# Optimization experiments

Hardware: AMD Instinct MI355X
Metric: run time of the kernel (lower is better)

The kernel has to match this reference:

```python
import jax, jax.numpy as jnp
import numpy as np

T, H, I, E, K = 4096, 2048, 1408, 8, 2


def setup_inputs() -> dict:
    key = jax.random.key(0)
    k1, k2, k3, k4, k5 = jax.random.split(key, 5)
    hidden_states = jax.random.normal(k1, (T, H), dtype=jnp.float32)
    w13 = jax.random.normal(k2, (E, 2 * I, H), dtype=jnp.float32) * 0.02
    w2 = jax.random.normal(k3, (E, H, I), dtype=jnp.float32) * 0.02
    topk_ids = jax.random.randint(k4, (T, K), 0, E, dtype=jnp.int32)
    topk_weights = jax.random.uniform(k5, (T, K), dtype=jnp.float32)
    return {
        "hidden_states": hidden_states,
        "w13": w13,
        "w2": w2,
        "topk_ids": topk_ids,
        "topk_weights": topk_weights,
    }


def reference(hidden_states, w13, w2, topk_ids, topk_weights):
    # hidden_states: [T, H]; w13: [E, 2I, H]; w2: [E, H, I]
    # topk_ids/topk_weights: [T, K]. local_expert_start = 0.
    num_tokens, hidden = hidden_states.shape
    num_experts = w13.shape[0]
    inter = w13.shape[1] // 2
    gate_w = w13[:, :inter, :]  # [E, I, H]
    up_w = w13[:, inter:, :]    # [E, I, H]

    # Dense per-expert gate/up projections (vectorized grouped GEMM).
    gate = jnp.einsum('th,eih->tei', hidden_states, gate_w)
    up = jnp.einsum('th,eih->tei', hidden_states, up_w)
    act = jax.nn.silu(gate) * up  # [T, E, I]

    # Scatter topk weights into a dense [T, E] routing matrix (zero elsewhere),
    # which reproduces the trivial impl's per-slot weighted accumulation.
    tok = jnp.arange(num_tokens, dtype=jnp.int32)[:, None]
    routing = jnp.zeros((num_tokens, num_experts), dtype=hidden_states.dtype)
    routing = routing.at[tok, topk_ids].add(topk_weights)

    # Weighted combine through the down projection; weighting act first avoids
    # materializing a [T, E, H] intermediate.
    act_w = act * routing[:, :, None]  # [T, E, I]
    out = jnp.einsum('tei,ehi->th', act_w, w2)  # [T, H]
    return out
```

## Files before the change

kernel.cpp:

```cpp
#include <hip/hip_runtime.h>
#include <hip/hip_bf16.h>

#define T_TOK 4096
#define HID   2048
#define INTER 1408
#define TWO_I 2816
#define NEXP  8
#define ROWCAP 9216

#define N8_HS  1048576
#define N8_W13 5767168
#define NCVT   ((N8_HS + N8_W13) / 256)

using bf16x8 = __attribute__((ext_vector_type(8))) __bf16;
using f32x4  = __attribute__((ext_vector_type(4))) float;

__device__ __forceinline__ unsigned short f2bf(float f) {
  unsigned u = __float_as_uint(f);
  u += 0x7fffu + ((u >> 16) & 1u);
  return (unsigned short)(u >> 16);
}

__device__ __forceinline__ void gload16(const void* g, void* l) {
  __builtin_amdgcn_global_load_lds(
      (const __attribute__((address_space(1))) void*)g,
      (__attribute__((address_space(3))) void*)l, 16, 0, 0);
}

__device__ __forceinline__ uint4 pack8(float4 a, float4 b) {
  union { unsigned short us[8]; uint4 v; } o;
  o.us[0] = f2bf(a.x); o.us[1] = f2bf(a.y); o.us[2] = f2bf(a.z); o.us[3] = f2bf(a.w);
  o.us[4] = f2bf(b.x); o.us[5] = f2bf(b.y); o.us[6] = f2bf(b.z); o.us[7] = f2bf(b.w);
  return o.v;
}

__global__ void cvt2route_kernel(const float* __restrict__ hs_f, unsigned short* __restrict__ hs_b,
                                 const float* __restrict__ w13_f, unsigned short* __restrict__ w13_b,
                                 const int* __restrict__ ids, const float* __restrict__ wts,
                                 float* __restrict__ R, int* __restrict__ counts) {
  int bid = blockIdx.x;
  if (bid >= NCVT) {
    int t = (bid - NCVT) * 256 + threadIdx.x;
    if (t >= T_TOK) return;
    int e0 = ids[t * 2], e1 = ids[t * 2 + 1];
    float w0 = wts[t * 2], w1 = wts[t * 2 + 1];
#pragma unroll
    for (int ee = 0; ee < NEXP; ++ee) {
      float r = (e0 == ee ? w0 : 0.0f) + (e1 == ee ? w1 : 0.0f);
      R[t * NEXP + ee] = r;
    }
    atomicAdd(&counts[e0], 1);
    if (e1 != e0) atomicAdd(&counts[e1], 1);
    return;
  }
  int i = bid * 256 + threadIdx.x;
  const float4* p;
  uint4* o;
  int j;
  if (i < N8_HS) {
    p = reinterpret_cast<const float4*>(hs_f);
    o = reinterpret_cast<uint4*>(hs_b);
    j = i;
  } else {
    p = reinterpret_cast<const float4*>(w13_f);
    o = reinterpret_cast<uint4*>(w13_b);
    j = i - N8_HS;
  }
  o[j] = pack8(p[j * 2], p[j * 2 + 1]);
}

__global__ void offsets_kernel(const int* __restrict__ counts,
                               int* __restrict__ offs, int* __restrict__ cursor,
                               int* __restrict__ tl) {
  if (threadIdx.x == 0) {
    int o = 0;
    for (int e = 0; e < NEXP; ++e) {
      offs[e] = o;
      cursor[e] = o;
      o += (counts[e] + 127) & ~127;
    }
    offs[NEXP] = o;
  }
  for (int i = threadIdx.x; i < ROWCAP; i += 256) tl[i] = -1;
}

__global__ void scatter_kernel(const int* __restrict__ ids,
                               int* __restrict__ cursor, int* __restrict__ tl,
                               int* __restrict__ inv) {
  int t = blockIdx.x * 256 + threadIdx.x;
  if (t >= T_TOK) return;
  int e0 = ids[t * 2], e1 = ids[t * 2 + 1];
  int p = atomicAdd(&cursor[e0], 1);
  tl[p] = t;
  inv[t * 2] = p;
  if (e1 != e0) {
    p = atomicAdd(&cursor[e1], 1);
    tl[p] = t;
    inv[t * 2 + 1] = p;
  } else {
    inv[t * 2 + 1] = -1;
  }
}

__global__ __launch_bounds__(256) void gemm1_kernel(
    const unsigned short* __restrict__ hs,
    const unsigned short* __restrict__ w13,
    unsigned short* __restrict__ act,
    const int* __restrict__ tl, const int* __restrict__ offs,
    const float* __restrict__ w2f, unsigned short* __restrict__ w2b) {
  const int tid = threadIdx.x;
  const int lin = blockIdx.x + 22 * (blockIdx.y + 32 * blockIdx.z);

  {
    const float4* p = reinterpret_cast<const float4*>(w2f);
    uint4* o = reinterpret_cast<uint4*>(w2b);
    int i0 = lin * 512 + tid;
    o[i0] = pack8(p[i0 * 2], p[i0 * 2 + 1]);
    int i1 = i0 + 256;
    o[i1] = pack8(p[i1 * 2], p[i1 * 2 + 1]);
  }

  const int work = (lin & 7) * 704 + (lin >> 3);
  const int bx = work % 22;
  const int by = (work / 22) & 31;
  const int bz = work / 704;

  const int e = bz;
  const int rbeg = offs[e], rend = offs[e + 1];
  const int m0 = rbeg + by * 128;
  if (m0 >= rend) return;
  const int n0 = bx * 64;

  __shared__ __align__(16) char smem[32768];

  const int lane = tid & 63, wave = tid >> 6;
  const int wm = wave >> 1, wn = wave & 1;
  const int srow = lane >> 3;
  const int scolswz = ((lane & 7) * 16) ^ (srow << 4);

  int atok[4];
#pragma unroll
  for (int it = 0; it < 4; ++it) {
    int tk = tl[m0 + it * 32 + wave * 8 + srow];
    atok[it] = tk < 0 ? 0 : tk;
  }

  const char* hs_b = (const char*)hs;
  const char* w13_b = (const char*)w13 + (size_t)e * (TWO_I * HID * 2);

  const char* asrc[4];
#pragma unroll
  for (int it = 0; it < 4; ++it)
    asrc[it] = hs_b + (size_t)atok[it] * (HID * 2) + scolswz;
  const char* gsrc[2]; const char* usrc[2];
#pragma unroll
  for (int it = 0; it < 2; ++it) {
    int row = it * 32 + wave * 8 + srow;
    gsrc[it] = w13_b + (size_t)(n0 + row) * (HID * 2) + scolswz;
    usrc[it] = w13_b + (size_t)(INTER + n0 + row) * (HID * 2) + scolswz;
  }

  const int ldsw = wave * 1024;
  const int rsw = (lane & 7) << 4;

  char* As = smem; char* Bg = smem + 16384; char* Bu = smem + 24576;

  f32x4 accg[4][2] = {};
  f32x4 accu[4][2] = {};

  for (int kt = 0; kt < HID / 64; ++kt) {
    const int kb = kt * 128;
#pragma unroll
    for (int it = 0; it < 4; ++it)
      gload16(asrc[it] + kb, As + it * 4096 + ldsw);
#pragma unroll
    for (int it = 0; it < 2; ++it) {
      gload16(gsrc[it] + kb, Bg + it * 4096 + ldsw);
      gload16(usrc[it] + kb, Bu + it * 4096 + ldsw);
    }
    __syncthreads();
#pragma unroll
    for (int kk = 0; kk < 2; ++kk) {
      const int ko = (kk * 64 + (lane >> 4) * 16) ^ rsw;
      bf16x8 a[4], bg[2], bu[2];
#pragma unroll
      for (int mi = 0; mi < 4; ++mi)
        a[mi] = *(const bf16x8*)(As + (wm * 64 + mi * 16 + (lane & 15)) * 128 + ko);
#pragma unroll
      for (int ni = 0; ni < 2; ++ni) {
        int r = wn * 32 + ni * 16 + (lane & 15);
        bg[ni] = *(const bf16x8*)(Bg + r * 128 + ko);
        bu[ni] = *(const bf16x8*)(Bu + r * 128 + ko);
      }
#pragma unroll
      for (int mi = 0; mi < 4; ++mi)
#pragma unroll
        for (int ni = 0; ni < 2; ++ni) {
          accg[mi][ni] = __builtin_amdgcn_mfma_f32_16x16x32_bf16(a[mi], bg[ni], accg[mi][ni], 0, 0, 0);
          accu[mi][ni] = __builtin_amdgcn_mfma_f32_16x16x32_bf16(a[mi], bu[ni], accu[mi][ni], 0, 0, 0);
        }
    }
    __syncthreads();
  }

#pragma unroll
  for (int mi = 0; mi < 4; ++mi)
#pragma unroll
    for (int j = 0; j < 4; ++j) {
      int rowL = wm * 64 + mi * 16 + (lane >> 4) * 4 + j;
      size_t base = (size_t)(m0 + rowL) * INTER + n0 + wn * 32;
#pragma unroll
      for (int ni = 0; ni < 2; ++ni) {
        float g = accg[mi][ni][j], u = accu[mi][ni][j];
        float s = (g / (1.0f + __expf(-g))) * u;
        act[base + ni * 16 + (lane & 15)] = f2bf(s);
      }
    }
}

__global__ __launch_bounds__(256) void gemm2_kernel(
    const unsigned short* __restrict__ act,
    const unsigned short* __restrict__ w2,
    const float* __restrict__ R, const int* __restrict__ tl,
    const int* __restrict__ offs, unsigned short* __restrict__ partial) {
  const int lin = blockIdx.x + 16 * (blockIdx.y + 32 * blockIdx.z);
  const int work = (lin & 7) * 512 + (lin >> 3);
  const int bx = work & 15;
  const int by = (work >> 4) & 31;
  const int bz = work >> 9;

  const int e = bz;
  const int rbeg = offs[e], rend = offs[e + 1];
  const int m0 = rbeg + by * 128;
  if (m0 >= rend) return;
  const int n0 = bx * 128;

  __shared__ __align__(16) char smem[32768];

  const int tid = threadIdx.x;
  const int lane = tid & 63, wave = tid >> 6;
  const int wm = wave >> 1, wn = wave & 1;
  const int srow = lane >> 3;
  const int scolswz = ((lane & 7) * 16) ^ (srow << 4);

  const char* act_b = (const char*)act;
  const char* w2_b = (const char*)w2 + (size_t)e * (HID * INTER * 2);

  const char* asrc[4]; const char* bsrc[4];
#pragma unroll
  for (int it = 0; it < 4; ++it) {
    int row = it * 32 + wave * 8 + srow;
    asrc[it] = act_b + (size_t)(m0 + row) * (INTER * 2) + scolswz;
    bsrc[it] = w2_b + (size_t)(n0 + row) * (INTER * 2) + scolswz;
  }

  const int ldsw = wave * 1024;
  const int rsw = (lane & 7) << 4;

  char* As = smem; char* Bs = smem + 16384;

  f32x4 acc[4][4] = {};

  for (int kt = 0; kt < INTER / 64; ++kt) {
    const int kb = kt * 128;
#pragma unroll
    for (int it = 0; it < 4; ++it) {
      gload16(asrc[it] + kb, As + it * 4096 + ldsw);
      gload16(bsrc[it] + kb, Bs + it * 4096 + ldsw);
    }
    __syncthreads();
#pragma unroll
    for (int kk = 0; kk < 2; ++kk) {
      const int ko = (kk * 64 + (lane >> 4) * 16) ^ rsw;
      bf16x8 a[4], b[4];
#pragma unroll
      for (int mi = 0; mi < 4; ++mi)
        a[mi] = *(const bf16x8*)(As + (wm * 64 + mi * 16 + (lane & 15)) * 128 + ko);
#pragma unroll
      for (int ni = 0; ni < 4; ++ni)
        b[ni] = *(const bf16x8*)(Bs + (wn * 64 + ni * 16 + (lane & 15)) * 128 + ko);
#pragma unroll
      for (int mi = 0; mi < 4; ++mi)
#pragma unroll
        for (int ni = 0; ni < 4; ++ni)
          acc[mi][ni] = __builtin_amdgcn_mfma_f32_16x16x32_bf16(a[mi], b[ni], acc[mi][ni], 0, 0, 0);
    }
    __syncthreads();
  }

#pragma unroll
  for (int mi = 0; mi < 4; ++mi) {
    float sc[4];
#pragma unroll
    for (int j = 0; j < 4; ++j) {
      int row = m0 + wm * 64 + mi * 16 + (lane >> 4) * 4 + j;
      int t = tl[row];
      sc[j] = t >= 0 ? R[t * NEXP + e] : 0.0f;
    }
#pragma unroll
    for (int ni = 0; ni < 4; ++ni) {
      int col = n0 + wn * 64 + ni * 16 + (lane & 15);
#pragma unroll
      for (int j = 0; j < 4; ++j) {
        int row = m0 + wm * 64 + mi * 16 + (lane >> 4) * 4 + j;
        partial[(size_t)row * HID + col] = f2bf(acc[mi][ni][j] * sc[j]);
      }
    }
  }
}

__global__ void combine_kernel(const unsigned short* __restrict__ P,
                               const int* __restrict__ inv,
                               float* __restrict__ out) {
  int idx = blockIdx.x * 256 + threadIdx.x;
  int t = idx >> 8;
  int c = (idx & 255) << 3;
  int p0 = inv[t * 2], p1 = inv[t * 2 + 1];
  union { uint4 v; unsigned short us[8]; } a, b;
  a.v = *(const uint4*)(P + (size_t)p0 * HID + c);
  float f[8];
#pragma unroll
  for (int j = 0; j < 8; ++j) f[j] = __uint_as_float((unsigned)a.us[j] << 16);
  if (p1 >= 0) {
    b.v = *(const uint4*)(P + (size_t)p1 * HID + c);
#pragma unroll
    for (int j = 0; j < 8; ++j) f[j] += __uint_as_float((unsigned)b.us[j] << 16);
  }
  float4 lo = {f[0], f[1], f[2], f[3]}, hi = {f[4], f[5], f[6], f[7]};
  *(float4*)(out + (size_t)t * HID + c) = lo;
  *(float4*)(out + (size_t)t * HID + c + 4) = hi;
}

extern "C" void kernel_launch(void* const* d_in, const int* in_sizes, int n_in,
                              void* d_out, int out_size, void* d_ws, size_t ws_size,
                              hipStream_t stream) {
  const float* hs_f  = (const float*)d_in[0];
  const float* w13_f = (const float*)d_in[1];
  const float* w2_f  = (const float*)d_in[2];
  const int*   ids   = (const int*)d_in[3];
  const float* wts   = (const float*)d_in[4];
  float* out = (float*)d_out;
  char* ws = (char*)d_ws;

  unsigned short* hs_b  = (unsigned short*)(ws);
  unsigned short* w13_b = (unsigned short*)(ws + 16777216);
  unsigned short* w2_b  = (unsigned short*)(ws + 109051904);
  unsigned short* act   = (unsigned short*)(ws + 155189248);
  float* R              = (float*)(ws + 181141504);
  int*   tl             = (int*)(ws + 181272576);
  int*   inv            = (int*)(ws + 181309440);
  int*   meta           = (int*)(ws + 181342208);
  unsigned short* partial = (unsigned short*)(ws + 16777216);
  int* counts = meta;
  int* offs   = meta + 8;
  int* cursor = meta + 17;

  hipMemsetAsync(meta, 0, 32 * sizeof(int), stream);

  cvt2route_kernel<<<dim3(NCVT + 16), dim3(256), 0, stream>>>(
      hs_f, hs_b, w13_f, w13_b, ids, wts, R, counts);

  offsets_kernel<<<dim3(1), dim3(256), 0, stream>>>(counts, offs, cursor, tl);
  scatter_kernel<<<dim3(T_TOK / 256), dim3(256), 0, stream>>>(ids, cursor, tl, inv);

  gemm1_kernel<<<dim3(22, 32, NEXP), dim3(256), 0, stream>>>(hs_b, w13_b, act, tl, offs, w2_f, w2_b);
  gemm2_kernel<<<dim3(16, 32, NEXP), dim3(256), 0, stream>>>(act, w2_b, R, tl, offs, partial);
  combine_kernel<<<dim3(T_TOK * (HID / 8) / 256), dim3(256), 0, stream>>>(partial, inv, out);
}
```

Baseline: 316.8 us.

## Rewrite grouped GEMMs as 256x256 tiles with 8-wave ping-pong LDS pipeline

Both grouped GEMM kernels move from 128-row tiles with 4 waves and a single LDS buffer to 256x256 output tiles with 8 waves. They use a double-buffered 128KB LDS and an eight-phase schedule that interleaves global-to-LDS loads with MFMA quadrants, using raw barriers, vmcnt waits and setprio. Gate and up rows are interleaved into one B tile so a single accumulator array holds both. The aim is to hide memory latency behind compute and raise arithmetic intensity per tile. In exchange, more rows are wasted on partially filled per-expert tiles, occupancy is limited by the large LDS footprint, and the hand-tuned barrier and waitcnt scheduling is fragile.

```diff
diff --git a/kernel.cpp b/kernel.cpp
--- a/kernel.cpp
+++ b/kernel.cpp
@@ -102,208 +102,270 @@
   }
 }
 
-__global__ __launch_bounds__(256) void gemm1_kernel(
+
+#define BARR do { __asm__ __volatile__("" ::: "memory"); \
+                  __builtin_amdgcn_s_barrier();           \
+                  __asm__ __volatile__("" ::: "memory"); } while (0)
+#define VMC(n) __asm__ __volatile__("s_waitcnt vmcnt(" #n ")" ::: "memory")
+
+#define STG(P, h, kt, slotOff, hOff)                                        \
+  do {                                                                      \
+    gload16(P[h][0] + (kt) * 128, smem + (slotOff) + (hOff) + chA);         \
+    gload16(P[h][1] + (kt) * 128, smem + (slotOff) + (hOff) + chA + 1024);  \
+  } while (0)
+
+#define LDA(dst, S, aq)                                                     \
+  do {                                                                      \
+    _Pragma("unroll") for (int mi = 0; mi < 4; ++mi) {                      \
+      const char* _p = smem + (S) + wmOff + ((aq) * 64 + mi * 16 + l15) * 128; \
+      dst[mi][0] = *(const bf16x8*)(_p + ko0);                              \
+      dst[mi][1] = *(const bf16x8*)(_p + ko1);                              \
+    }                                                                       \
+  } while (0)
+
+#define LDB(dst, S, bq)                                                     \
+  do {                                                                      \
+    _Pragma("unroll") for (int ni = 0; ni < 2; ++ni) {                      \
+      const char* _p = smem + (S) + 32768 + wnhOff +                        \
+                       (wn1 * 64 + ((bq) * 2 + ni) * 16 + l15) * 128;       \
+      dst[ni][0] = *(const bf16x8*)(_p + ko0);                              \
+      dst[ni][1] = *(const bf16x8*)(_p + ko1);                              \
+    }                                                                       \
+  } while (0)
+
+#define MFQ(A, B, aq, bq)                                                   \
+  do {                                                                      \
+    __builtin_amdgcn_s_setprio(1);                                          \
+    _Pragma("unroll") for (int mi = 0; mi < 4; ++mi)                        \
+    _Pragma("unroll") for (int ni = 0; ni < 2; ++ni) {                      \
+      acc[(aq) * 4 + mi][(bq) * 2 + ni] = __builtin_amdgcn_mfma_f32_16x16x32_bf16( \
+          A[mi][0], B[ni][0], acc[(aq) * 4 + mi][(bq) * 2 + ni], 0, 0, 0);  \
+      acc[(aq) * 4 + mi][(bq) * 2 + ni] = __builtin_amdgcn_mfma_f32_16x16x32_bf16( \
+          A[mi][1], B[ni][1], acc[(aq) * 4 + mi][(bq) * 2 + ni], 0, 0, 0);  \
+    }                                                                       \
+    __builtin_amdgcn_s_setprio(0);                                          \
+  } while (0)
+
+#define EIGHT_PHASES(NIT_, NL_LIM_)                                         \
+  for (int i = 0; i < (NIT_); ++i) {                                        \
+    const int t0 = 2 * i, t1 = t0 + 1;                                      \
+    const bool nl = (i < (NL_LIM_));                                        \
+                                                                    \
+    LDA(a_lo, 0, 0);                                                        \
+    LDB(b_lo, 0, 0);                                                        \
+    STG(aS, 0, t1, 65536, 0);                                               \
+    BARR; MFQ(a_lo, b_lo, 0, 0); BARR;                                      \
+                                                                    \
+    LDB(b_hi, 0, 1);                                                        \
+    STG(aS, 1, t1, 65536, 16384);                                           \
+    BARR; MFQ(a_lo, b_hi, 0, 1); BARR;                                      \
+                                                                    \
+    LDA(a_hi, 0, 1);                                                        \
+    if (nl) STG(bS, 0, t0 + 2, 0, 32768);                                   \
+    BARR; MFQ(a_hi, b_hi, 1, 1); BARR;                                      \
+                                                                    \
+    if (nl) STG(bS, 1, t0 + 2, 0, 49152);                                   \
+    BARR; MFQ(a_hi, b_lo, 1, 0);                                            \
+    if (nl) { VMC(4); } else { VMC(0); }                                    \
+    BARR;                                                                   \
+                                                                    \
+    LDA(a_lo, 65536, 0);                                                    \
+    LDB(b_lo, 65536, 0);                                                    \
+    if (nl) STG(aS, 0, t0 + 2, 0, 0);                                       \
+    BARR; MFQ(a_lo, b_lo, 0, 0); BARR;                                      \
+                                                                    \
+    LDB(b_hi, 65536, 1);                                                    \
+    if (nl) STG(aS, 1, t0 + 2, 0, 16384);                                   \
+    BARR; MFQ(a_lo, b_hi, 0, 1); BARR;                                      \
+                                                                    \
+    LDA(a_hi, 65536, 1);                                                    \
+    if (nl) STG(bS, 0, t1 + 2, 65536, 32768);                               \
+    BARR; MFQ(a_hi, b_hi, 1, 1); BARR;                                      \
+                                                                    \
+    if (nl) STG(bS, 1, t1 + 2, 65536, 49152);                               \
+    BARR; MFQ(a_hi, b_lo, 1, 0);                                            \
+    if (nl) VMC(4);                                                         \
+    BARR;                                                                   \
+  }
+
+#define PROLOGUE_STAGE()                                                    \
+  do {                                                                      \
+    STG(aS, 0, 0, 0, 0);                                                    \
+    STG(aS, 1, 0, 0, 16384);                                                \
+    STG(bS, 0, 0, 0, 32768);                                                \
+    STG(bS, 1, 0, 0, 49152);                                                \
+    STG(bS, 0, 1, 65536, 32768);                                            \
+    STG(bS, 1, 1, 65536, 49152);                                            \
+    VMC(4);                                                                 \
+    BARR;                                                                   \
+  } while (0)
+
+__global__ __launch_bounds__(512, 2) void gemm1_kernel(
     const unsigned short* __restrict__ hs,
     const unsigned short* __restrict__ w13,
     unsigned short* __restrict__ act,
     const int* __restrict__ tl, const int* __restrict__ offs,
     const float* __restrict__ w2f, unsigned short* __restrict__ w2b) {
   const int tid = threadIdx.x;
-  const int lin = blockIdx.x + 22 * (blockIdx.y + 32 * blockIdx.z);
+  const int lin = blockIdx.x + 11 * (blockIdx.y + 16 * blockIdx.z);
 
   {
     const float4* p = reinterpret_cast<const float4*>(w2f);
     uint4* o = reinterpret_cast<uint4*>(w2b);
-    int i0 = lin * 512 + tid;
-    o[i0] = pack8(p[i0 * 2], p[i0 * 2 + 1]);
-    int i1 = i0 + 256;
-    o[i1] = pack8(p[i1 * 2], p[i1 * 2 + 1]);
-  }
-
-  const int work = (lin & 7) * 704 + (lin >> 3);
-  const int bx = work % 22;
-  const int by = (work / 22) & 31;
-  const int bz = work / 704;
+    int gid = lin * 512 + tid;
+#pragma unroll
+    for (int q = 0; q < 4; ++q) {
+      int idx = q * 720896 + gid;
+      o[idx] = pack8(p[idx * 2], p[idx * 2 + 1]);
+    }
+  }
+
+  const int work = (lin & 7) * 176 + (lin >> 3);
+  const int bz = work / 176;
+  const int rem = work - bz * 176;
+  const int bx = rem % 11;
+  const int by = rem / 11;
 
   const int e = bz;
   const int rbeg = offs[e], rend = offs[e + 1];
-  const int m0 = rbeg + by * 128;
+  const int m0 = rbeg + by * 256;
   if (m0 >= rend) return;
-  const int n0 = bx * 64;
-
-  __shared__ __align__(16) char smem[32768];
+  const int n0 = bx * 128;
+
+  __shared__ __align__(16) char smem[131072];
 
   const int lane = tid & 63, wave = tid >> 6;
-  const int wm = wave >> 1, wn = wave & 1;
+  const int wm = wave >> 2, wn = wave & 3;
+  const int l15 = lane & 15;
   const int srow = lane >> 3;
   const int scolswz = ((lane & 7) * 16) ^ (srow << 4);
-
-  int atok[4];
-#pragma unroll
-  for (int it = 0; it < 4; ++it) {
-    int tk = tl[m0 + it * 32 + wave * 8 + srow];
-    atok[it] = tk < 0 ? 0 : tk;
-  }
+  const int chA = wave * 2048;
+  const int wmOff = wm * 16384;
+  const int wnhOff = (wn >> 1) * 16384;
+  const int wn1 = wn & 1;
+  const int rsw = (lane & 7) << 4;
+  const int ko0 = ((lane >> 4) * 16) ^ rsw;
+  const int ko1 = (64 + (lane >> 4) * 16) ^ rsw;
 
   const char* hs_b = (const char*)hs;
   const char* w13_b = (const char*)w13 + (size_t)e * (TWO_I * HID * 2);
 
-  const char* asrc[4];
-#pragma unroll
-  for (int it = 0; it < 4; ++it)
-    asrc[it] = hs_b + (size_t)atok[it] * (HID * 2) + scolswz;
-  const char* gsrc[2]; const char* usrc[2];
-#pragma unroll
-  for (int it = 0; it < 2; ++it) {
-    int row = it * 32 + wave * 8 + srow;
-    gsrc[it] = w13_b + (size_t)(n0 + row) * (HID * 2) + scolswz;
-    usrc[it] = w13_b + (size_t)(INTER + n0 + row) * (HID * 2) + scolswz;
-  }
-
-  const int ldsw = wave * 1024;
-  const int rsw = (lane & 7) << 4;
-
-  char* As = smem; char* Bg = smem + 16384; char* Bu = smem + 24576;
-
-  f32x4 accg[4][2] = {};
-  f32x4 accu[4][2] = {};
-
-  for (int kt = 0; kt < HID / 64; ++kt) {
-    const int kb = kt * 128;
-#pragma unroll
-    for (int it = 0; it < 4; ++it)
-      gload16(asrc[it] + kb, As + it * 4096 + ldsw);
+  const char* aS[2][2];
+  const char* bS[2][2];
+#pragma unroll
+  for (int h = 0; h < 2; ++h)
 #pragma unroll
     for (int it = 0; it < 2; ++it) {
-      gload16(gsrc[it] + kb, Bg + it * 4096 + ldsw);
-      gload16(usrc[it] + kb, Bu + it * 4096 + ldsw);
-    }
-    __syncthreads();
-#pragma unroll
-    for (int kk = 0; kk < 2; ++kk) {
-      const int ko = (kk * 64 + (lane >> 4) * 16) ^ rsw;
-      bf16x8 a[4], bg[2], bu[2];
-#pragma unroll
-      for (int mi = 0; mi < 4; ++mi)
-        a[mi] = *(const bf16x8*)(As + (wm * 64 + mi * 16 + (lane & 15)) * 128 + ko);
-#pragma unroll
-      for (int ni = 0; ni < 2; ++ni) {
-        int r = wn * 32 + ni * 16 + (lane & 15);
-        bg[ni] = *(const bf16x8*)(Bg + r * 128 + ko);
-        bu[ni] = *(const bf16x8*)(Bu + r * 128 + ko);
+      int rl = h * 128 + (wave * 2 + it) * 8 + srow;
+      int grow = m0 + rl;
+      int tk = (grow < rend) ? tl[grow] : 0;
+      if (tk < 0) tk = 0;
+      aS[h][it] = hs_b + (size_t)tk * 4096 + scolswz;
+      int wg = rl >> 6, sub = rl & 63;
+      int srcB = (sub < 32) ? (n0 + wg * 32 + sub)
+                            : (INTER + n0 + wg * 32 + (sub - 32));
+      bS[h][it] = w13_b + (size_t)srcB * 4096 + scolswz;
+    }
+
+  f32x4 acc[8][4] = {};
+  bf16x8 a_lo[4][2], a_hi[4][2], b_lo[2][2], b_hi[2][2];
+
+  PROLOGUE_STAGE();
+  EIGHT_PHASES(16, 15);
+
+  const bool okst = (wm == 0) || (rend - m0 >= 256);
+  if (okst) {
+#pragma unroll
+    for (int MI = 0; MI < 8; ++MI)
+#pragma unroll
+      for (int j = 0; j < 4; ++j) {
+        int row = m0 + wm * 128 + MI * 16 + (lane >> 4) * 4 + j;
+        size_t base = (size_t)row * INTER + n0 + wn * 32;
+#pragma unroll
+        for (int NI = 0; NI < 2; ++NI) {
+          float g = acc[MI][NI][j], u = acc[MI][NI + 2][j];
+          float s = (g / (1.0f + __expf(-g))) * u;
+          act[base + NI * 16 + l15] = f2bf(s);
+        }
       }
-#pragma unroll
-      for (int mi = 0; mi < 4; ++mi)
-#pragma unroll
-        for (int ni = 0; ni < 2; ++ni) {
-          accg[mi][ni] = __builtin_amdgcn_mfma_f32_16x16x32_bf16(a[mi], bg[ni], accg[mi][ni], 0, 0, 0);
-          accu[mi][ni] = __builtin_amdgcn_mfma_f32_16x16x32_bf16(a[mi], bu[ni], accu[mi][ni], 0, 0, 0);
-        }
-    }
-    __syncthreads();
-  }
-
-#pragma unroll
-  for (int mi = 0; mi < 4; ++mi)
-#pragma unroll
-    for (int j = 0; j < 4; ++j) {
-      int rowL = wm * 64 + mi * 16 + (lane >> 4) * 4 + j;
-      size_t base = (size_t)(m0 + rowL) * INTER + n0 + wn * 32;
-#pragma unroll
-      for (int ni = 0; ni < 2; ++ni) {
-        float g = accg[mi][ni][j], u = accu[mi][ni][j];
-        float s = (g / (1.0f + __expf(-g))) * u;
-        act[base + ni * 16 + (lane & 15)] = f2bf(s);
-      }
-    }
-}
-
-__global__ __launch_bounds__(256) void gemm2_kernel(
+  }
+}
+
+__global__ __launch_bounds__(512, 2) void gemm2_kernel(
     const unsigned short* __restrict__ act,
     const unsigned short* __restrict__ w2,
     const float* __restrict__ R, const int* __restrict__ tl,
     const int* __restrict__ offs, unsigned short* __restrict__ partial) {
-  const int lin = blockIdx.x + 16 * (blockIdx.y + 32 * blockIdx.z);
-  const int work = (lin & 7) * 512 + (lin >> 3);
-  const int bx = work & 15;
-  const int by = (work >> 4) & 31;
-  const int bz = work >> 9;
+  const int tid = threadIdx.x;
+  const int lin = blockIdx.x + 8 * (blockIdx.y + 16 * blockIdx.z);
+  const int work = (lin & 7) * 128 + (lin >> 3);
+  const int bz = work >> 7;
+  const int rem = work & 127;
+  const int bx = rem & 7;
+  const int by = rem >> 3;
 
   const int e = bz;
   const int rbeg = offs[e], rend = offs[e + 1];
-  const int m0 = rbeg + by * 128;
+  const int m0 = rbeg + by * 256;
   if (m0 >= rend) return;
-  const int n0 = bx * 128;
-
-  __shared__ __align__(16) char smem[32768];
-
-  const int tid = threadIdx.x;
+  const int n0 = bx * 256;
+
+  __shared__ __align__(16) char smem[131072];
+
   const int lane = tid & 63, wave = tid >> 6;
-  const int wm = wave >> 1, wn = wave & 1;
+  const int wm = wave >> 2, wn = wave & 3;
+  const int l15 = lane & 15;
   const int srow = lane >> 3;
   const int scolswz = ((lane & 7) * 16) ^ (srow << 4);
+  const int chA = wave * 2048;
+  const int wmOff = wm * 16384;
+  const int wnhOff = (wn >> 1) * 16384;
+  const int wn1 = wn & 1;
+  const int rsw = (lane & 7) << 4;
+  const int ko0 = ((lane >> 4) * 16) ^ rsw;
+  const int ko1 = (64 + (lane >> 4) * 16) ^ rsw;
 
   const char* act_b = (const char*)act;
   const char* w2_b = (const char*)w2 + (size_t)e * (HID * INTER * 2);
 
-  const char* asrc[4]; const char* bsrc[4];
-#pragma unroll
-  for (int it = 0; it < 4; ++it) {
-    int row = it * 32 + wave * 8 + srow;
-    asrc[it] = act_b + (size_t)(m0 + row) * (INTER * 2) + scolswz;
-    bsrc[it] = w2_b + (size_t)(n0 + row) * (INTER * 2) + scolswz;
-  }
-
-  const int ldsw = wave * 1024;
-  const int rsw = (lane & 7) << 4;
-
-  char* As = smem; char* Bs = smem + 16384;
-
-  f32x4 acc[4][4] = {};
-
-  for (int kt = 0; kt < INTER / 64; ++kt) {
-    const int kb = kt * 128;
-#pragma unroll
-    for (int it = 0; it < 4; ++it) {
-      gload16(asrc[it] + kb, As + it * 4096 + ldsw);
-      gload16(bsrc[it] + kb, Bs + it * 4096 + ldsw);
-    }
-    __syncthreads();
-#pragma unroll
-    for (int kk = 0; kk < 2; ++kk) {
-      const int ko = (kk * 64 + (lane >> 4) * 16) ^ rsw;
-      bf16x8 a[4], b[4];
-#pragma unroll
-      for (int mi = 0; mi < 4; ++mi)
-        a[mi] = *(const bf16x8*)(As + (wm * 64 + mi * 16 + (lane & 15)) * 128 + ko);
-#pragma unroll
-      for (int ni = 0; ni < 4; ++ni)
-        b[ni] = *(const bf16x8*)(Bs + (wn * 64 + ni * 16 + (lane & 15)) * 128 + ko);
-#pragma unroll
-      for (int mi = 0; mi < 4; ++mi)
-#pragma unroll
-        for (int ni = 0; ni < 4; ++ni)
-          acc[mi][ni] = __builtin_amdgcn_mfma_f32_16x16x32_bf16(a[mi], b[ni], acc[mi][ni], 0, 0, 0);
-    }
-    __syncthreads();
-  }
-
-#pragma unroll
-  for (int mi = 0; mi < 4; ++mi) {
-    float sc[4];
-#pragma unroll
-    for (int j = 0; j < 4; ++j) {
-      int row = m0 + wm * 64 + mi * 16 + (lane >> 4) * 4 + j;
-      int t = tl[row];
-      sc[j] = t >= 0 ? R[t * NEXP + e] : 0.0f;
-    }
-#pragma unroll
-    for (int ni = 0; ni < 4; ++ni) {
-      int col = n0 + wn * 64 + ni * 16 + (lane & 15);
+  const char* aS[2][2];
+  const char* bS[2][2];
+#pragma unroll
+  for (int h = 0; h < 2; ++h)
+#pragma unroll
+    for (int it = 0; it < 2; ++it) {
+      int rl = h * 128 + (wave * 2 + it) * 8 + srow;
+      int grow = m0 + rl;
+      if (grow >= rend) grow = rbeg;
+      aS[h][it] = act_b + (size_t)grow * (INTER * 2) + scolswz;
+      bS[h][it] = w2_b + (size_t)(n0 + rl) * (INTER * 2) + scolswz;
+    }
+
+  f32x4 acc[8][4] = {};
+  bf16x8 a_lo[4][2], a_hi[4][2], b_lo[2][2], b_hi[2][2];
+
+  PROLOGUE_STAGE();
+  EIGHT_PHASES(11, 10);
+
+  const bool okst = (wm == 0) || (rend - m0 >= 256);
+  if (okst) {
+#pragma unroll
+    for (int MI = 0; MI < 8; ++MI) {
+      float sc[4];
 #pragma unroll
       for (int j = 0; j < 4; ++j) {
-        int row = m0 + wm * 64 + mi * 16 + (lane >> 4) * 4 + j;
-        partial[(size_t)row * HID + col] = f2bf(acc[mi][ni][j] * sc[j]);
+        int row = m0 + wm * 128 + MI * 16 + (lane >> 4) * 4 + j;
+        int t = tl[row];
+        sc[j] = t >= 0 ? R[t * NEXP + e] : 0.0f;
+      }
+#pragma unroll
+      for (int NI = 0; NI < 4; ++NI) {
+        int col = n0 + wn * 64 + NI * 16 + l15;
+#pragma unroll
+        for (int j = 0; j < 4; ++j) {
+          int row = m0 + wm * 128 + MI * 16 + (lane >> 4) * 4 + j;
+          partial[(size_t)row * HID + col] = f2bf(acc[MI][NI][j] * sc[j]);
+        }
       }
     }
   }
@@ -363,7 +425,7 @@
   offsets_kernel<<<dim3(1), dim3(256), 0, stream>>>(counts, offs, cursor, tl);
   scatter_kernel<<<dim3(T_TOK / 256), dim3(256), 0, stream>>>(ids, cursor, tl, inv);
 
-  gemm1_kernel<<<dim3(22, 32, NEXP), dim3(256), 0, stream>>>(hs_b, w13_b, act, tl, offs, w2_f, w2_b);
-  gemm2_kernel<<<dim3(16, 32, NEXP), dim3(256), 0, stream>>>(act, w2_b, R, tl, offs, partial);
+  gemm1_kernel<<<dim3(11, 16, 8), dim3(512), 0, stream>>>(hs_b, w13_b, act, tl, offs, w2_f, w2_b);
+  gemm2_kernel<<<dim3(8, 16, 8), dim3(512), 0, stream>>>(act, w2_b, R, tl, offs, partial);
   combine_kernel<<<dim3(T_TOK * (HID / 8) / 256), dim3(256), 0, stream>>>(partial, inv, out);
 }
```

Measured after the change: 299.6 us (median of 3 runs). 1.06x faster.
